# Kernel optimization log

Hardware: AMD Instinct MI355X
Metric: run time of the kernel (lower is better)

## Reference

```python
import jax, jax.numpy as jnp
import numpy as np

EPS = 1e-8

def _ste(x, q):
    # straight-through estimator: forward = q, backward = identity
    return x + jax.lax.stop_gradient(q - x)

def quant_act_uint8(x):
    # per-tensor uint8 activation fake-quant (Brevitas Uint8ActPerTensorFloat style)
    s = jax.lax.stop_gradient(jnp.maximum(jnp.max(x), EPS)) / 255.0
    q = jnp.clip(jnp.round(x / s), 0.0, 255.0) * s
    return _ste(x, q), s

def quant_weight_int8_perchannel(w):
    # per-output-channel symmetric int8 fake-quant; w: [out, in]
    s = jax.lax.stop_gradient(jnp.maximum(jnp.max(jnp.abs(w), axis=1, keepdims=True), EPS)) / 127.0
    q = jnp.clip(jnp.round(w / s), -128.0, 127.0) * s
    return _ste(w, q), s[:, 0]

def quant_bias_int32(b, s_in, s_w):
    # bias quantized at scale s_in * s_w[c] (Brevitas Int32Bias)
    s = jax.lax.stop_gradient(s_in * s_w)
    q = jnp.round(b / s) * s
    return _ste(b, q)

def quant_linear(x, w, b):
    xq, s_in = quant_act_uint8(x)
    wq, s_w = quant_weight_int8_perchannel(w)
    bq = quant_bias_int32(b, s_in, s_w)
    return jnp.einsum('btd,fd->btf', xq, wq) + bq

def setup_inputs() -> dict:
    key = jax.random.key(0)
    k1, k2, k3, k4, k5 = jax.random.split(key, 5)
    B, S, D, F = 4, 2048, 1024, 4096
    return {
        'x': jax.random.normal(k1, (B, S, D), dtype=jnp.float32),
        'w1': jax.random.normal(k2, (F, D), dtype=jnp.float32) * (1.0 / np.sqrt(D)),
        'b1': jax.random.normal(k3, (F,), dtype=jnp.float32) * 0.01,
        'w2': jax.random.normal(k4, (D, F), dtype=jnp.float32) * (1.0 / np.sqrt(F)),
        'b2': jax.random.normal(k5, (D,), dtype=jnp.float32) * 0.01,
    }

def reference(x, w1, b1, w2, b2):
    h = jax.nn.relu(quant_linear(x, w1, b1))
    # dropout is identity in eval mode
    return quant_linear(h, w2, b2)
```

## Files before the change

### kernel.cpp

```cpp
#include <hip/hip_runtime.h>
#include <stdint.h>

#define EPSQ 1e-8f

typedef __attribute__((ext_vector_type(4))) int i32x4;

__device__ __forceinline__ unsigned enc_f(float f) {
    unsigned u = __float_as_uint(f);
    return (u & 0x80000000u) ? ~u : (u | 0x80000000u);
}
__device__ __forceinline__ float dec_f(unsigned u) {
    return (u & 0x80000000u) ? __uint_as_float(u & 0x7fffffffu)
                             : __uint_as_float(~u);
}

__device__ __forceinline__ float wave_max_f(float v) {
    #pragma unroll
    for (int off = 32; off; off >>= 1) v = fmaxf(v, __shfl_xor(v, off));
    return v;
}
__device__ __forceinline__ int wave_sum_i(int v) {
    #pragma unroll
    for (int off = 32; off; off >>= 1) v += __shfl_xor(v, off);
    return v;
}

__global__ __launch_bounds__(256) void k_prep(
    const float4* __restrict__ x, long n4x, float* __restrict__ partials,
    const float* __restrict__ w1, signed char* __restrict__ w1q,
    float* __restrict__ sw1, int* __restrict__ rs1,
    const float* __restrict__ w2, signed char* __restrict__ w2q,
    float* __restrict__ sw2, int* __restrict__ rs2) {
    __shared__ float sm[4];
    __shared__ int   si[4];
    int b = blockIdx.x;
    int wid = threadIdx.x >> 6;
    if (b < 2048) {
        long i = (long)b * 256 + threadIdx.x;
        float m = -3.4e38f;
        for (; i < n4x; i += 2048L * 256) {
            float4 v = x[i];
            m = fmaxf(fmaxf(m, fmaxf(v.x, v.y)), fmaxf(v.z, v.w));
        }
        m = wave_max_f(m);
        if ((threadIdx.x & 63) == 0) sm[wid] = m;
        __syncthreads();
        if (threadIdx.x == 0)
            partials[b] = fmaxf(fmaxf(sm[0], sm[1]), fmaxf(sm[2], sm[3]));
        return;
    }
    const float* w; signed char* q; float* s_out; int* rs_out; int row, L;
    if (b < 2048 + 4096) { row = b - 2048; w = w1; q = w1q; s_out = sw1; rs_out = rs1; L = 1024; }
    else                 { row = b - 6144; w = w2; q = w2q; s_out = sw2; rs_out = rs2; L = 4096; }

    const float4* wr = (const float4*)(w + (long)row * L);
    int n4 = L >> 2;
    float m = 0.0f;
    for (int i = threadIdx.x; i < n4; i += 256) {
        float4 v = wr[i];
        m = fmaxf(m, fmaxf(fmaxf(fabsf(v.x), fabsf(v.y)),
                           fmaxf(fabsf(v.z), fabsf(v.w))));
    }
    m = wave_max_f(m);
    if ((threadIdx.x & 63) == 0) sm[wid] = m;
    __syncthreads();
    m = fmaxf(fmaxf(sm[0], sm[1]), fmaxf(sm[2], sm[3]));
    float s = fmaxf(m, EPSQ) / 127.0f;

    char4* qr = (char4*)(q + (long)row * L);
    int isum = 0;
    for (int i = threadIdx.x; i < n4; i += 256) {
        float4 v = wr[i];
        int a = min(max((int)rintf(v.x / s), -128), 127);
        int bb = min(max((int)rintf(v.y / s), -128), 127);
        int c = min(max((int)rintf(v.z / s), -128), 127);
        int d = min(max((int)rintf(v.w / s), -128), 127);
        isum += a + bb + c + d;
        char4 cc; cc.x = (char)a; cc.y = (char)bb; cc.z = (char)c; cc.w = (char)d;
        qr[i] = cc;
    }
    isum = wave_sum_i(isum);
    if ((threadIdx.x & 63) == 0) si[wid] = isum;
    __syncthreads();
    if (threadIdx.x == 0) {
        s_out[row]  = s;
        rs_out[row] = si[0] + si[1] + si[2] + si[3];
    }
}

__global__ __launch_bounds__(256) void k_quant_act(
    const float4* __restrict__ in, char4* __restrict__ out, long n4,
    const float* __restrict__ partials, unsigned* __restrict__ slots) {
    __shared__ float sm[4];
    float m = -3.4e38f;
    for (int i = threadIdx.x; i < 2048; i += 256) m = fmaxf(m, partials[i]);
    m = wave_max_f(m);
    if ((threadIdx.x & 63) == 0) sm[threadIdx.x >> 6] = m;
    __syncthreads();
    m = fmaxf(fmaxf(sm[0], sm[1]), fmaxf(sm[2], sm[3]));
    if (blockIdx.x == 0 && threadIdx.x == 0) {
        slots[0] = enc_f(m);
        slots[1] = 0u;
    }
    float s = fmaxf(m, EPSQ) / 255.0f;
    long i = (long)blockIdx.x * 256 + threadIdx.x;
    for (; i < n4; i += (long)gridDim.x * 256) {
        float4 v = in[i];
        int a = min(max((int)rintf(v.x / s), 0), 255) - 128;
        int b = min(max((int)rintf(v.y / s), 0), 255) - 128;
        int c = min(max((int)rintf(v.z / s), 0), 255) - 128;
        int d = min(max((int)rintf(v.w / s), 0), 255) - 128;
        char4 cc; cc.x = (char)a; cc.y = (char)b; cc.z = (char)c; cc.w = (char)d;
        out[i] = cc;
    }
}

__global__ __launch_bounds__(256) void k_requant(
    const ushort4* __restrict__ h16, char4* __restrict__ hq,
    const float* __restrict__ sblk, const unsigned* __restrict__ slots, long n4) {
    float s_h = fmaxf(dec_f(slots[1]), EPSQ) / 255.0f;
    float inv = 1.0f / (65535.0f * s_h);
    long i = (long)blockIdx.x * 256 + threadIdx.x;
    for (; i < n4; i += (long)gridDim.x * 256) {
        long e = i << 2;
        int m = (int)(e >> 12);
        int f = (int)(e & 4095);
        float fq = sblk[(m >> 8) * 32 + (f >> 7)] * inv;
        ushort4 u = h16[i];
        char4 cc;
        cc.x = (char)(min(max((int)rintf(u.x * fq), 0), 255) - 128);
        cc.y = (char)(min(max((int)rintf(u.y * fq), 0), 255) - 128);
        cc.z = (char)(min(max((int)rintf(u.z * fq), 0), 255) - 128);
        cc.w = (char)(min(max((int)rintf(u.w * fq), 0), 255) - 128);
        hq[i] = cc;
    }
}

__device__ __forceinline__ void gl_lds16(const signed char* g, signed char* l) {
    __builtin_amdgcn_global_load_lds(
        (const __attribute__((address_space(1))) unsigned int*)g,
        (__attribute__((address_space(3))) unsigned int*)l, 16, 0, 0);
}

template<int MODE, int BM, int NW>
__global__ __launch_bounds__(NW * 64, (MODE == 0 ? 3 : 4)) void k_gemm_i8(
    const signed char* __restrict__ A,
    const signed char* __restrict__ B,
    const float* __restrict__ s_w,
    const int* __restrict__ rowsum,
    const float* __restrict__ bias,
    const unsigned* __restrict__ act_slot,
    float* __restrict__ Cf,
    unsigned short* __restrict__ H16,
    float* __restrict__ sblk,
    unsigned* __restrict__ omax_slot,
    int M, int N, long K) {
    __shared__ __align__(16) signed char Als[BM * 128];
    __shared__ __align__(16) signed char Bls[128 * 128];
    __shared__ float red[NW];

    const int t    = threadIdx.x;
    const int lane = t & 63;
    const int w    = t >> 6;
    const int m0   = blockIdx.y * BM;
    const int n0   = blockIdx.x * 128;
    const int mr   = lane & 15;
    const int qq   = lane >> 4;
    constexpr int PB = 8 / NW;

    const signed char* a0 = A + (long)(m0 + w * 32 + mr) * K + qq * 16;
    const signed char* b0 = B + (long)(n0 + w * PB * 16 + mr) * K + qq * 16;
    signed char* ad = Als + w * 4096 + lane * 16;
    signed char* bd = Bls + w * PB * 2048 + lane * 16;

    const int wrow = (w >> 1) * 64;
    const int wcol = (w & 1) * 64;
    const int a_base = (w >> 1) * 8192 + lane * 16;
    const int b_base = (w & 1) * 8192 + lane * 16;

    i32x4 acc[4][4];
    #pragma unroll
    for (int i = 0; i < 4; i++)
        #pragma unroll
        for (int j = 0; j < 4; j++) acc[i][j] = (i32x4){0, 0, 0, 0};

    for (long k0 = 0; k0 < K; k0 += 128) {
        __syncthreads();
        gl_lds16(a0 + k0,               ad);
        gl_lds16(a0 + k0 + 64,          ad + 1024);
        gl_lds16(a0 + k0 + 16 * K,      ad + 2048);
        gl_lds16(a0 + k0 + 16 * K + 64, ad + 3072);
        #pragma unroll
        for (int p = 0; p < PB; p++) {
            gl_lds16(b0 + k0 + (long)p * 16 * K,      bd + p * 2048);
            gl_lds16(b0 + k0 + (long)p * 16 * K + 64, bd + p * 2048 + 1024);
        }
        __syncthreads();

        #pragma unroll
        for (int kk = 0; kk < 2; kk++) {
            i32x4 af[4], bf[4];
            #pragma unroll
            for (int i = 0; i < 4; i++)
                af[i] = *(const i32x4*)(Als + a_base + i * 2048 + kk * 1024);
            #pragma unroll
            for (int j = 0; j < 4; j++)
                bf[j] = *(const i32x4*)(Bls + b_base + j * 2048 + kk * 1024);
            #pragma unroll
            for (int i = 0; i < 4; i++)
                #pragma unroll
                for (int j = 0; j < 4; j++)
                    acc[i][j] = __builtin_amdgcn_mfma_i32_16x16x64_i8(
                        af[i], bf[j], acc[i][j], 0, 0, 0);
        }
    }

    const float s_act = fmaxf(dec_f(*act_slot), EPSQ) / 255.0f;

    if (MODE == 3) {
        float sscv[4], bintv[4]; int icorv[4];
        float lmax = 0.0f;
        #pragma unroll
        for (int j = 0; j < 4; j++) {
            int gn = n0 + wcol + j * 16 + mr;
            float ssc  = s_act * s_w[gn];
            float bint = rintf(bias[gn] / ssc);
            int   icor = 128 * rowsum[gn];
            sscv[j] = ssc; bintv[j] = bint; icorv[j] = icor;
            int im = -2147483647 - 1;
            #pragma unroll
            for (int i = 0; i < 4; i++)
                #pragma unroll
                for (int r = 0; r < 4; r++) im = max(im, acc[i][j][r]);
            lmax = fmaxf(lmax, ssc * ((float)(im + icor) + bint));
        }
        lmax = fmaxf(lmax, 0.0f);
        lmax = wave_max_f(lmax);
        if (lane == 0) red[w] = lmax;
        __syncthreads();
        float bm = red[0];
        #pragma unroll
        for (int i = 1; i < NW; i++) bm = fmaxf(bm, red[i]);
        if (t == 0) {
            sblk[blockIdx.y * gridDim.x + blockIdx.x] = bm;
            atomicMax(omax_slot, enc_f(bm));
        }
        float inv = 65535.0f / fmaxf(bm, EPSQ);
        #pragma unroll
        for (int j = 0; j < 4; j++) {
            int gn = n0 + wcol + j * 16 + mr;
            #pragma unroll
            for (int i = 0; i < 4; i++) {
                #pragma unroll
                for (int r = 0; r < 4; r++) {
                    int gm = m0 + wrow + i * 16 + qq * 4 + r;
                    float h = fmaxf(
                        sscv[j] * ((float)(acc[i][j][r] + icorv[j]) + bintv[j]),
                        0.0f);
                    int u = min((int)rintf(h * inv), 65535);
                    H16[(long)gm * N + gn] = (unsigned short)u;
                }
            }
        }
        return;
    }

    #pragma unroll
    for (int j = 0; j < 4; j++) {
        int gn = n0 + wcol + j * 16 + mr;
        float ssc  = s_act * s_w[gn];
        float bint = rintf(bias[gn] / ssc);
        int   icor = 128 * rowsum[gn];
        #pragma unroll
        for (int i = 0; i < 4; i++) {
            #pragma unroll
            for (int r = 0; r < 4; r++) {
                int gm = m0 + wrow + i * 16 + qq * 4 + r;
                Cf[(long)gm * N + gn] =
                    ssc * ((float)(acc[i][j][r] + icor) + bint);
            }
        }
    }
}

extern "C" void kernel_launch(void* const* d_in, const int* in_sizes, int n_in,
                              void* d_out, int out_size, void* d_ws, size_t ws_size,
                              hipStream_t stream) {
    const float* x  = (const float*)d_in[0];
    const float* w1 = (const float*)d_in[1];
    const float* b1 = (const float*)d_in[2];
    const float* w2 = (const float*)d_in[3];
    const float* b2 = (const float*)d_in[4];
    float* out = (float*)d_out;

    const int M = 8192, D = 1024, F = 4096;

    char* ws = (char*)d_ws;
    size_t off = 0;
    unsigned* slots = (unsigned*)ws;               off += 256;
    float* partials = (float*)(ws + off);          off += 2048 * 4;
    signed char* xi  = (signed char*)(ws + off);   off += (size_t)M * D;
    signed char* w1q = (signed char*)(ws + off);   off += (size_t)F * D;
    signed char* w2q = (signed char*)(ws + off);   off += (size_t)D * F;
    float* sw1 = (float*)(ws + off);               off += (size_t)F * 4;
    float* sw2 = (float*)(ws + off);               off += (size_t)D * 4;
    int* rs1   = (int*)(ws + off);                 off += (size_t)F * 4;
    int* rs2   = (int*)(ws + off);                 off += (size_t)D * 4;
    signed char* hq = (signed char*)(ws + off);    off += (size_t)M * F;
    unsigned short* h16 = (unsigned short*)(ws + off); off += (size_t)M * F * 2;
    float* sblk = (float*)(ws + off);              off += 1024 * 4;

    k_prep<<<dim3(2048 + F + D), dim3(256), 0, stream>>>(
        (const float4*)x, (long)M * D / 4, partials,
        w1, w1q, sw1, rs1, w2, w2q, sw2, rs2);
    k_quant_act<<<dim3(2048), dim3(256), 0, stream>>>(
        (const float4*)x, (char4*)xi, (long)M * D / 4, partials, slots);
    k_gemm_i8<3, 256, 8><<<dim3(F / 128, M / 256), dim3(512), 0, stream>>>(
        xi, w1q, sw1, rs1, b1, slots + 0, nullptr, h16, sblk, slots + 1,
        M, F, (long)D);
    k_requant<<<dim3(2048), dim3(256), 0, stream>>>(
        (const ushort4*)h16, (char4*)hq, sblk, slots, (long)M * F / 4);
    k_gemm_i8<0, 128, 4><<<dim3(D / 128, M / 128), dim3(256), 0, stream>>>(
        hq, w2q, sw2, rs2, b2, slots + 1, out, nullptr, nullptr, nullptr,
        M, D, (long)F);

    (void)in_sizes; (void)n_in; (void)out_size; (void)ws_size;
}
```

Measured before the change: 274.1 us.

## Stage GEMM epilogue through LDS for coalesced stores and swizzle workgroup order

```diff
diff --git a/kernel.cpp b/kernel.cpp
--- a/kernel.cpp
+++ b/kernel.cpp
@@ -155,23 +155,29 @@
     float* __restrict__ sblk,
     unsigned* __restrict__ omax_slot,
     int M, int N, long K) {
-    __shared__ __align__(16) signed char Als[BM * 128];
-    __shared__ __align__(16) signed char Bls[128 * 128];
+    constexpr int ASZ = BM * 128;
+    constexpr int BSZ = 128 * 128;
+    __shared__ __align__(16) signed char SH[ASZ + BSZ];
     __shared__ float red[NW];
 
     const int t    = threadIdx.x;
     const int lane = t & 63;
     const int w    = t >> 6;
-    const int m0   = blockIdx.y * BM;
-    const int n0   = blockIdx.x * 128;
+    const unsigned nwg = gridDim.x * gridDim.y;
+    const unsigned wg  = blockIdx.y * gridDim.x + blockIdx.x;
+    const unsigned swg = (wg & 7u) * (nwg >> 3) + (wg >> 3);
+    const int bx = (int)(swg % gridDim.x);
+    const int by = (int)(swg / gridDim.x);
+    const int m0 = by * BM;
+    const int n0 = bx * 128;
     const int mr   = lane & 15;
     const int qq   = lane >> 4;
     constexpr int PB = 8 / NW;
 
     const signed char* a0 = A + (long)(m0 + w * 32 + mr) * K + qq * 16;
     const signed char* b0 = B + (long)(n0 + w * PB * 16 + mr) * K + qq * 16;
-    signed char* ad = Als + w * 4096 + lane * 16;
-    signed char* bd = Bls + w * PB * 2048 + lane * 16;
+    signed char* ad = SH + w * 4096 + lane * 16;
+    signed char* bd = SH + ASZ + w * PB * 2048 + lane * 16;
 
     const int wrow = (w >> 1) * 64;
     const int wcol = (w & 1) * 64;
@@ -202,10 +208,10 @@
             i32x4 af[4], bf[4];
             #pragma unroll
             for (int i = 0; i < 4; i++)
-                af[i] = *(const i32x4*)(Als + a_base + i * 2048 + kk * 1024);
+                af[i] = *(const i32x4*)(SH + a_base + i * 2048 + kk * 1024);
             #pragma unroll
             for (int j = 0; j < 4; j++)
-                bf[j] = *(const i32x4*)(Bls + b_base + j * 2048 + kk * 1024);
+                bf[j] = *(const i32x4*)(SH + ASZ + b_base + j * 2048 + kk * 1024);
             #pragma unroll
             for (int i = 0; i < 4; i++)
                 #pragma unroll
@@ -217,68 +223,101 @@
 
     const float s_act = fmaxf(dec_f(*act_slot), EPSQ) / 255.0f;
 
+    float sscv[4], bintv[4]; int icorv[4];
+    #pragma unroll
+    for (int j = 0; j < 4; j++) {
+        int gn = n0 + wcol + j * 16 + mr;
+        sscv[j]  = s_act * s_w[gn];
+        bintv[j] = rintf(bias[gn] / sscv[j]);
+        icorv[j] = 128 * rowsum[gn];
+    }
+
     if (MODE == 3) {
-        float sscv[4], bintv[4]; int icorv[4];
         float lmax = 0.0f;
         #pragma unroll
         for (int j = 0; j < 4; j++) {
-            int gn = n0 + wcol + j * 16 + mr;
-            float ssc  = s_act * s_w[gn];
-            float bint = rintf(bias[gn] / ssc);
-            int   icor = 128 * rowsum[gn];
-            sscv[j] = ssc; bintv[j] = bint; icorv[j] = icor;
             int im = -2147483647 - 1;
             #pragma unroll
             for (int i = 0; i < 4; i++)
                 #pragma unroll
                 for (int r = 0; r < 4; r++) im = max(im, acc[i][j][r]);
-            lmax = fmaxf(lmax, ssc * ((float)(im + icor) + bint));
-        }
-        lmax = fmaxf(lmax, 0.0f);
-        lmax = wave_max_f(lmax);
+            lmax = fmaxf(lmax, sscv[j] * ((float)(im + icorv[j]) + bintv[j]));
+        }
+        lmax = wave_max_f(fmaxf(lmax, 0.0f));
         if (lane == 0) red[w] = lmax;
         __syncthreads();
         float bm = red[0];
         #pragma unroll
         for (int i = 1; i < NW; i++) bm = fmaxf(bm, red[i]);
         if (t == 0) {
-            sblk[blockIdx.y * gridDim.x + blockIdx.x] = bm;
+            sblk[by * gridDim.x + bx] = bm;
             atomicMax(omax_slot, enc_f(bm));
         }
         float inv = 65535.0f / fmaxf(bm, EPSQ);
-        #pragma unroll
-        for (int j = 0; j < 4; j++) {
-            int gn = n0 + wcol + j * 16 + mr;
-            #pragma unroll
-            for (int i = 0; i < 4; i++) {
+
+        unsigned short* tile = (unsigned short*)SH;
+        #pragma unroll
+        for (int ph = 0; ph < 2; ++ph) {
+            if ((w >> 2) == ph) {
+                int rbase = wrow & 127;
                 #pragma unroll
-                for (int r = 0; r < 4; r++) {
-                    int gm = m0 + wrow + i * 16 + qq * 4 + r;
-                    float h = fmaxf(
-                        sscv[j] * ((float)(acc[i][j][r] + icorv[j]) + bintv[j]),
-                        0.0f);
-                    int u = min((int)rintf(h * inv), 65535);
-                    H16[(long)gm * N + gn] = (unsigned short)u;
+                for (int j = 0; j < 4; j++) {
+                    int cg = ((wcol + j * 16) >> 4) ^ qq;
+                    #pragma unroll
+                    for (int i = 0; i < 4; i++) {
+                        #pragma unroll
+                        for (int r = 0; r < 4; r++) {
+                            int lrl = rbase + i * 16 + qq * 4 + r;
+                            float h = fmaxf(
+                                sscv[j] * ((float)(acc[i][j][r] + icorv[j]) + bintv[j]),
+                                0.0f);
+                            int u = min((int)rintf(h * inv), 65535);
+                            tile[lrl * 128 + cg * 16 + mr] = (unsigned short)u;
+                        }
+                    }
                 }
             }
+            __syncthreads();
+            int tr = t >> 4, tc = t & 15;
+            int cp = tc ^ (((tr >> 2) & 3) << 1);
+            #pragma unroll
+            for (int it = 0; it < 4; ++it) {
+                int lrl = it * 32 + tr;
+                i32x4 v = *(const i32x4*)(tile + lrl * 128 + cp * 8);
+                *(i32x4*)(H16 + (long)(m0 + ph * 128 + lrl) * N + n0 + tc * 8) = v;
+            }
+            if (ph == 0) __syncthreads();
         }
         return;
     }
 
-    #pragma unroll
-    for (int j = 0; j < 4; j++) {
-        int gn = n0 + wcol + j * 16 + mr;
-        float ssc  = s_act * s_w[gn];
-        float bint = rintf(bias[gn] / ssc);
-        int   icor = 128 * rowsum[gn];
-        #pragma unroll
-        for (int i = 0; i < 4; i++) {
-            #pragma unroll
-            for (int r = 0; r < 4; r++) {
-                int gm = m0 + wrow + i * 16 + qq * 4 + r;
-                Cf[(long)gm * N + gn] =
-                    ssc * ((float)(acc[i][j][r] + icor) + bint);
+    float* tf = (float*)SH;
+    #pragma unroll
+    for (int ph = 0; ph < 2; ++ph) {
+        __syncthreads();
+        if ((w >> 1) == ph) {
+            #pragma unroll
+            for (int j = 0; j < 4; j++) {
+                int cg = ((wcol + j * 16) >> 4) ^ qq;
+                #pragma unroll
+                for (int i = 0; i < 4; i++) {
+                    #pragma unroll
+                    for (int r = 0; r < 4; r++) {
+                        int lrl = i * 16 + qq * 4 + r;
+                        tf[lrl * 128 + cg * 16 + mr] =
+                            sscv[j] * ((float)(acc[i][j][r] + icorv[j]) + bintv[j]);
+                    }
+                }
             }
+        }
+        __syncthreads();
+        int tr = t >> 5, tc = t & 31;
+        #pragma unroll
+        for (int it = 0; it < 8; ++it) {
+            int lrl = it * 8 + tr;
+            int sz = (lrl >> 2) & 3;
+            i32x4 v = *(const i32x4*)(tf + lrl * 128 + (tc ^ (sz << 2)) * 4);
+            *(i32x4*)(Cf + (long)(m0 + ph * 64 + lrl) * N + n0 + tc * 4) = v;
         }
     }
 }
```

New measurement: 272.8 us (median of 3 runs). Within noise of the previous version (-0.5%).
